# Kernel optimization log

Measured on AMD Instinct MI355X. Metric: run time of the kernel, lower is better.

Reference implementation:

```python
import jax, jax.numpy as jnp
import numpy as np

G, M, K = 4096, 50, 30          # graphs, nodes per graph, sort-pool k
H, NUM_LAYERS, F_IN = 32, 3, 128
DEG = 8
N = G * M
E = N * DEG
D_LAT = H * NUM_LAYERS + 1       # 97 = conv1d kernel/stride
DENSE_DIM = (((K - 2) // 2 + 1) - 5 + 1) * 32  # 352


def setup_inputs() -> dict:
    key = jax.random.key(0)
    ks = jax.random.split(key, 14)
    x = jax.random.normal(ks[0], (N, F_IN), dtype=jnp.float32)
    # graph-local random edges so each subgraph is self-contained
    offs = (jnp.arange(E, dtype=jnp.int32) // (M * DEG)) * M
    src = jax.random.randint(ks[1], (E,), 0, M, dtype=jnp.int32) + offs
    dst = jax.random.randint(ks[2], (E,), 0, M, dtype=jnp.int32) + offs
    edge_index = jnp.stack([src, dst])
    batch = jnp.repeat(jnp.arange(G, dtype=jnp.int32), M)

    def lin(k, i, o):
        return (jax.random.normal(k, (i, o), dtype=jnp.float32) / np.sqrt(i)).astype(jnp.float32)

    W0, b0 = lin(ks[3], F_IN, H), jnp.zeros((H,), jnp.float32)
    W1, b1 = lin(ks[4], H, H), jnp.zeros((H,), jnp.float32)
    W2, b2 = lin(ks[5], H, H), jnp.zeros((H,), jnp.float32)
    W3, b3 = lin(ks[6], H, 1), jnp.zeros((1,), jnp.float32)
    C1w = (jax.random.normal(ks[7], (16, 1, D_LAT)) / np.sqrt(D_LAT)).astype(jnp.float32)
    C1b = jnp.zeros((16,), jnp.float32)
    C2w = (jax.random.normal(ks[8], (32, 16, 5)) / np.sqrt(16 * 5)).astype(jnp.float32)
    C2b = jnp.zeros((32,), jnp.float32)
    L1w, L1b = lin(ks[9], DENSE_DIM, 128), jnp.zeros((128,), jnp.float32)
    L2w, L2b = lin(ks[10], 128, 1), jnp.zeros((1,), jnp.float32)
    return {"x": x, "edge_index": edge_index, "batch": batch,
            "W0": W0, "b0": b0, "W1": W1, "b1": b1, "W2": W2, "b2": b2,
            "W3": W3, "b3": b3, "C1w": C1w, "C1b": C1b, "C2w": C2w, "C2b": C2b,
            "L1w": L1w, "L1b": L1b, "L2w": L2w, "L2b": L2b}


def _gcn_norm(edge_index, n):
    # add self loops, symmetric normalization (PyG GCNConv default)
    loop = jnp.arange(n, dtype=edge_index.dtype)
    src = jnp.concatenate([edge_index[0], loop])
    dst = jnp.concatenate([edge_index[1], loop])
    deg = jax.ops.segment_sum(jnp.ones_like(dst, dtype=jnp.float32), dst, num_segments=n)
    dinv = jnp.where(deg > 0, deg ** -0.5, 0.0)
    return src, dst, dinv[src] * dinv[dst]


def _gcn_conv(h, W, b, src, dst, norm, n):
    h = h @ W                                    # [N, out]
    msg = h[src] * norm[:, None]                 # gather + weight
    return jax.ops.segment_sum(msg, dst, num_segments=n) + b


def reference(x, edge_index, batch, W0, b0, W1, b1, W2, b2, W3, b3,
              C1w, C1b, C2w, C2b, L1w, L1b, L2w, L2b):
    n = x.shape[0]
    src, dst, norm = _gcn_norm(edge_index, n)
    h1 = jnp.tanh(_gcn_conv(x, W0, b0, src, dst, norm, n))
    h2 = jnp.tanh(_gcn_conv(h1, W1, b1, src, dst, norm, n))
    h3 = jnp.tanh(_gcn_conv(h2, W2, b2, src, dst, norm, n))
    h4 = jnp.tanh(_gcn_conv(h3, W3, b3, src, dst, norm, n))
    lat = jnp.concatenate([h1, h2, h3, h4], axis=-1)      # [N, 97]
    # global_sort_pool: graphs are contiguous equal-size blocks (batch = arange(G).repeat(M)),
    # sort nodes within each graph by last channel, descending, keep top K
    xd = lat.reshape(G, M, D_LAT)
    order = jnp.argsort(-xd[..., -1], axis=1)             # [G, M]
    xs = jnp.take_along_axis(xd, order[..., None], axis=1)[:, :K]  # [G, K, 97]
    # Conv1d(1,16,97,stride=97) on [G,1,K*97] == per-slot linear over the 97 latent dims
    z = jnp.einsum('gtd,cd->gct', xs, C1w[:, 0, :]) + C1b[None, :, None]  # [G,16,K]
    z = jax.nn.relu(z)
    z = z.reshape(G, 16, K // 2, 2).max(axis=-1)          # MaxPool1d(2,2) -> [G,16,15]
    z = jax.lax.conv_general_dilated(z, C2w, window_strides=(1,), padding='VALID',
                                     dimension_numbers=('NCH', 'OIH', 'NCH'))
    z = jax.nn.relu(z + C2b[None, :, None])               # [G,32,11]
    z = z.reshape(G, -1)                                  # [G,352]
    z = jax.nn.relu(z @ L1w + L1b)
    # dropout: eval mode (identity)
    return z @ L2w + L2b                                  # [G,1]
```

## Files before the change

### kernel.cpp

```cpp
#include <hip/hip_runtime.h>
#include <math.h>

#define NG 4096
#define M 50
#define KTOP 30
#define H 32
#define F_IN 128
#define EPG 400
#define PADE 552
#define E_TOTAL (NG * EPG)
#define DLAT 97
#define LATS 100
#define NTHREADS 256
#define WS_C1P 0
#define XH 64

__device__ __forceinline__ float fast_tanh(float x) {
    x = fminf(fmaxf(x, -15.f), 15.f);
    float e = __expf(2.f * x);
    return 1.f - 2.f / (e + 1.f);
}

__global__ void prep_kernel(const float* __restrict__ C1w, float* __restrict__ ws) {
    const int tid = blockIdx.x * blockDim.x + threadIdx.x;
    if (tid < 1600) {
        int c = tid / 100, d = tid - c * 100;
        ws[WS_C1P + tid] = (d < DLAT) ? C1w[c * DLAT + d] : 0.f;
    }
}

template <int KIN>
__device__ __forceinline__ void gcn_matmul_acc(const float* hin, int istride,
                                               const float* __restrict__ W,
                                               const int* rows, float* acc, int j) {
#pragma unroll 2
    for (int k4 = 0; k4 < KIN / 4; k4++) {
        const float w0 = W[(4 * k4 + 0) * H + j];
        const float w1 = W[(4 * k4 + 1) * H + j];
        const float w2 = W[(4 * k4 + 2) * H + j];
        const float w3 = W[(4 * k4 + 3) * H + j];
#pragma unroll
        for (int r = 0; r < 7; r++) {
            const float4 xv = *(const float4*)(hin + rows[r] * istride + 4 * k4);
            acc[r] += xv.x * w0 + xv.y * w1 + xv.z * w2 + xv.w * w3;
        }
    }
}

template <int KIN>
__device__ __forceinline__ void gcn_matmul(const float* hin, int istride,
                                           const float* __restrict__ W,
                                           float (*tb)[H], int tid) {
    const int j = tid & 31, iset = tid >> 5;
    float acc[7];
    int rows[7];
#pragma unroll
    for (int r = 0; r < 7; r++) {
        acc[r] = 0.f;
        int i = iset + r * 8;
        rows[r] = (i >= M) ? (M - 1) : i;
    }
    gcn_matmul_acc<KIN>(hin, istride, W, rows, acc, j);
#pragma unroll
    for (int r = 0; r < 7; r++) {
        int i = iset + r * 8;
        if (i < M) tb[i][j] = acc[r];
    }
}

__device__ __forceinline__ void gcn_agg(const float (*tbuf)[H], const float* __restrict__ b,
                                        float (*lat)[LATS], int col0,
                                        const float* dinv, const unsigned short* csr_off,
                                        const unsigned char* csr_src, const float* csr_nrm,
                                        int tid) {
    const int j = tid & 31, iset = tid >> 5;
    for (int i = iset; i < M; i += 8) {
        float acc = tbuf[i][j] * dinv[i] * dinv[i];
        int e0 = csr_off[i], e1 = csr_off[i + 1];
        for (int e = e0; e < e1; e += 4) {
            unsigned sp = *(const unsigned*)(csr_src + e);
            float4 nr = *(const float4*)(csr_nrm + e);
            acc += tbuf[sp & 255][j] * nr.x;
            acc += tbuf[(sp >> 8) & 255][j] * nr.y;
            acc += tbuf[(sp >> 16) & 255][j] * nr.z;
            acc += tbuf[sp >> 24][j] * nr.w;
        }
        lat[i][col0 + j] = fast_tanh(acc + b[j]);
    }
}

struct Post {
    float pbuf[16][15];
    union {
        struct { float z1[16][KTOP]; unsigned char ord[52]; } a;
        struct { float z2[352]; float red[256]; } b;
    } u;
};

__global__ __launch_bounds__(NTHREADS, 4)
void dgcnn_kernel(const float* __restrict__ x, const int* __restrict__ eidx,
                  const float* __restrict__ ws,
                  const float* __restrict__ W0, const float* __restrict__ b0,
                  const float* __restrict__ W1, const float* __restrict__ b1,
                  const float* __restrict__ W2, const float* __restrict__ b2,
                  const float* __restrict__ W3, const float* __restrict__ b3,
                  const float* __restrict__ C1b,
                  const float* __restrict__ C2w, const float* __restrict__ C2b,
                  const float* __restrict__ L1w, const float* __restrict__ L1b,
                  const float* __restrict__ L2w, const float* __restrict__ L2b,
                  float* __restrict__ out) {
    __shared__ __align__(16) union Big {
        float xs[M][XH];
        float lat[M][LATS];
    } big;
    __shared__ __align__(16) union TP {
        float tbuf[M][H];
        Post post;
    } tp;
    __shared__ __align__(16) float csr_nrm[PADE];
    __shared__ unsigned char csr_src[PADE];
    __shared__ unsigned short csr_off[M + 2];
    __shared__ int   degi[M];
    __shared__ float dinv[M];

    const int g = blockIdx.x;
    const int tid = threadIdx.x;
    const int nbase = g * M;
    const int ebase = g * EPG;

    {
        const float4* xg4 = (const float4*)(x + (size_t)nbase * F_IN);
        float4* xs4 = (float4*)big.xs;
        for (int idx = tid; idx < M * XH / 4; idx += NTHREADS) {
            int i = idx >> 4, q = idx & 15;
            xs4[idx] = xg4[i * 32 + q];
        }
    }
    if (tid < M) degi[tid] = 1;
    for (int idx = tid; idx < PADE; idx += NTHREADS) {
        csr_nrm[idx] = 0.f;
        csr_src[idx] = 0;
    }
    __syncthreads();
    for (int e = tid; e < EPG; e += NTHREADS) {
        int d = eidx[E_TOTAL + ebase + e] - nbase;
        atomicAdd(&degi[d], 1);
    }
    __syncthreads();
    if (tid < M) dinv[tid] = rsqrtf((float)degi[tid]);
    if (tid < 64) {
        int cnt  = (tid < M) ? (degi[tid] - 1) : 0;
        int cntp = (cnt + 3) & ~3;
        int incl = cntp;
#pragma unroll
        for (int off = 1; off < 64; off <<= 1) {
            int nv = __shfl_up(incl, off);
            if (tid >= off) incl += nv;
        }
        if (tid < M) {
            csr_off[tid] = (unsigned short)(incl - cntp);
            degi[tid] = incl - cntp;
        }
        if (tid == M - 1) csr_off[M] = (unsigned short)incl;
    }
    __syncthreads();
    const int j1 = tid & 31, iset1 = tid >> 5;
    float acc1[7];
    int rows1[7];
#pragma unroll
    for (int r = 0; r < 7; r++) {
        acc1[r] = 0.f;
        int i = iset1 + r * 8;
        rows1[r] = (i >= M) ? (M - 1) : i;
    }
    for (int e = tid; e < EPG; e += NTHREADS) {
        int s = eidx[ebase + e] - nbase;
        int d = eidx[E_TOTAL + ebase + e] - nbase;
        float nr = dinv[s] * dinv[d];
        int pos = atomicAdd(&degi[d], 1);
        csr_src[pos] = (unsigned char)s;
        csr_nrm[pos] = nr;
    }
    gcn_matmul_acc<XH>(&big.xs[0][0], XH, W0, rows1, acc1, j1);
    __syncthreads();
    {
        const float4* xg4 = (const float4*)(x + (size_t)nbase * F_IN);
        float4* xs4 = (float4*)big.xs;
        for (int idx = tid; idx < M * XH / 4; idx += NTHREADS) {
            int i = idx >> 4, q = idx & 15;
            xs4[idx] = xg4[i * 32 + 16 + q];
        }
    }
    __syncthreads();
    gcn_matmul_acc<XH>(&big.xs[0][0], XH, W0 + XH * H, rows1, acc1, j1);
#pragma unroll
    for (int r = 0; r < 7; r++) {
        int i = iset1 + r * 8;
        if (i < M) tp.tbuf[i][j1] = acc1[r];
    }
    __syncthreads();

    gcn_agg(tp.tbuf, b0, big.lat, 0, dinv, csr_off, csr_src, csr_nrm, tid);
    for (int idx = tid; idx < 3 * M; idx += NTHREADS)
        big.lat[idx / 3][DLAT + idx % 3] = 0.f;
    __syncthreads();
    gcn_matmul<H>(&big.lat[0][0], LATS, W1, tp.tbuf, tid);
    __syncthreads();
    gcn_agg(tp.tbuf, b1, big.lat, 32, dinv, csr_off, csr_src, csr_nrm, tid);
    __syncthreads();
    gcn_matmul<H>(&big.lat[0][32], LATS, W2, tp.tbuf, tid);
    __syncthreads();
    gcn_agg(tp.tbuf, b2, big.lat, 64, dinv, csr_off, csr_src, csr_nrm, tid);
    __syncthreads();
    if (tid < M) {
        float acc = 0.f;
        for (int k = 0; k < H; k++) acc += big.lat[tid][64 + k] * W3[k];
        tp.tbuf[tid][0] = acc;
    }
    __syncthreads();
    if (tid < M) {
        float acc = tp.tbuf[tid][0] * dinv[tid] * dinv[tid];
        int e0 = csr_off[tid], e1 = csr_off[tid + 1];
        for (int e = e0; e < e1; e += 4) {
            unsigned sp = *(const unsigned*)(csr_src + e);
            float4 nr = *(const float4*)(csr_nrm + e);
            acc += tp.tbuf[sp & 255][0] * nr.x + tp.tbuf[(sp >> 8) & 255][0] * nr.y
                 + tp.tbuf[(sp >> 16) & 255][0] * nr.z + tp.tbuf[sp >> 24][0] * nr.w;
        }
        big.lat[tid][96] = tanhf(acc + b3[0]);
    }
    __syncthreads();

    if (tid < M) {
        float v = big.lat[tid][96];
        int r = 0;
        for (int jj = 0; jj < M; jj++) {
            float vj = big.lat[jj][96];
            r += (vj > v) || (vj == v && jj < tid);
        }
        tp.post.u.a.ord[r] = (unsigned char)tid;
    }
    __syncthreads();

    for (int idx = tid; idx < 16 * KTOP; idx += NTHREADS) {
        int t = idx >> 4, c = idx & 15;
        const float4* row = (const float4*)big.lat[tp.post.u.a.ord[t]];
        const float4* cw  = (const float4*)(ws + WS_C1P + c * LATS);
        float acc = 0.f;
#pragma unroll 5
        for (int q = 0; q < LATS / 4; q++) {
            float4 rv = row[q], wv = cw[q];
            acc += rv.x * wv.x + rv.y * wv.y + rv.z * wv.z + rv.w * wv.w;
        }
        tp.post.u.a.z1[c][t] = fmaxf(acc + C1b[c], 0.f);
    }
    __syncthreads();

    for (int idx = tid; idx < 16 * 15; idx += NTHREADS) {
        int c = idx / 15, t = idx - c * 15;
        tp.post.pbuf[c][t] = fmaxf(tp.post.u.a.z1[c][2 * t],
                                   tp.post.u.a.z1[c][2 * t + 1]);
    }
    __syncthreads();

    for (int idx = tid; idx < 352; idx += NTHREADS) {
        int o = idx / 11, t = idx - o * 11;
        float acc = C2b[o];
        for (int i = 0; i < 16; i++) {
#pragma unroll
            for (int k = 0; k < 5; k++)
                acc += tp.post.pbuf[i][t + k] * C2w[(o * 16 + i) * 5 + k];
        }
        tp.post.u.b.z2[idx] = fmaxf(acc, 0.f);
    }
    __syncthreads();

    {
        int jj = tid & 127, half = tid >> 7;
        float acc = (half == 0) ? L1b[jj] : 0.f;
        int f0 = half * 176;
        for (int f = f0; f < f0 + 176; f++)
            acc += tp.post.u.b.z2[f] * L1w[f * 128 + jj];
        tp.post.u.b.red[tid] = acc;
    }
    __syncthreads();
    if (tid < 128)
        tp.post.u.b.red[tid] =
            fmaxf(tp.post.u.b.red[tid] + tp.post.u.b.red[tid + 128], 0.f)
            * L2w[tid];
    __syncthreads();
    if (tid < 64) {
        float v = tp.post.u.b.red[tid] + tp.post.u.b.red[tid + 64];
#pragma unroll
        for (int off = 32; off >= 1; off >>= 1)
            v += __shfl_down(v, off);
        if (tid == 0) out[g] = v + L2b[0];
    }
}

extern "C" void kernel_launch(void* const* d_in, const int* in_sizes, int n_in,
                              void* d_out, int out_size, void* d_ws, size_t ws_size,
                              hipStream_t stream) {
    const float* x    = (const float*)d_in[0];
    const int*   eidx = (const int*)d_in[1];
    float* ws = (float*)d_ws;
    prep_kernel<<<7, 256, 0, stream>>>((const float*)d_in[11], ws);
    dgcnn_kernel<<<NG, NTHREADS, 0, stream>>>(
        x, eidx, ws,
        (const float*)d_in[3],  (const float*)d_in[4],
        (const float*)d_in[5],  (const float*)d_in[6],
        (const float*)d_in[7],  (const float*)d_in[8],
        (const float*)d_in[9],  (const float*)d_in[10],
        (const float*)d_in[12],
        (const float*)d_in[13], (const float*)d_in[14],
        (const float*)d_in[15], (const float*)d_in[16],
        (const float*)d_in[17], (const float*)d_in[18],
        (float*)d_out);
}
```

Measured before the change: 376.7 us.

## Factor GCN normalization into row scaling and drop per-edge norm array

Rewrites the symmetric GCN normalization so each source row is pre-scaled by dinv after the matmul and the aggregated sum is scaled by dinv of the destination. This removes the per-edge csr_nrm shared array, its initialization and float4 loads, and the per-edge multiplies in aggregation. Padding edges now point to an extra zero row (index 50) of tbuf, which enlarges tbuf by one row. Rounding order changes slightly.

```diff
diff --git a/kernel.cpp b/kernel.cpp
--- a/kernel.cpp
+++ b/kernel.cpp
@@ -50,7 +50,7 @@
 template <int KIN>
 __device__ __forceinline__ void gcn_matmul(const float* hin, int istride,
                                            const float* __restrict__ W,
-                                           float (*tb)[H], int tid) {
+                                           float (*tb)[H], const float* dinv, int tid) {
     const int j = tid & 31, iset = tid >> 5;
     float acc[7];
     int rows[7];
@@ -64,28 +64,26 @@
 #pragma unroll
     for (int r = 0; r < 7; r++) {
         int i = iset + r * 8;
-        if (i < M) tb[i][j] = acc[r];
+        if (i < M) tb[i][j] = acc[r] * dinv[i];
     }
 }
 
 __device__ __forceinline__ void gcn_agg(const float (*tbuf)[H], const float* __restrict__ b,
                                         float (*lat)[LATS], int col0,
                                         const float* dinv, const unsigned short* csr_off,
-                                        const unsigned char* csr_src, const float* csr_nrm,
-                                        int tid) {
+                                        const unsigned char* csr_src, int tid) {
     const int j = tid & 31, iset = tid >> 5;
     for (int i = iset; i < M; i += 8) {
-        float acc = tbuf[i][j] * dinv[i] * dinv[i];
+        float acc = tbuf[i][j];
         int e0 = csr_off[i], e1 = csr_off[i + 1];
         for (int e = e0; e < e1; e += 4) {
             unsigned sp = *(const unsigned*)(csr_src + e);
-            float4 nr = *(const float4*)(csr_nrm + e);
-            acc += tbuf[sp & 255][j] * nr.x;
-            acc += tbuf[(sp >> 8) & 255][j] * nr.y;
-            acc += tbuf[(sp >> 16) & 255][j] * nr.z;
-            acc += tbuf[sp >> 24][j] * nr.w;
-        }
-        lat[i][col0 + j] = fast_tanh(acc + b[j]);
+            acc += tbuf[sp & 255][j];
+            acc += tbuf[(sp >> 8) & 255][j];
+            acc += tbuf[(sp >> 16) & 255][j];
+            acc += tbuf[sp >> 24][j];
+        }
+        lat[i][col0 + j] = fast_tanh(acc * dinv[i] + b[j]);
     }
 }
 
@@ -114,10 +112,9 @@
         float lat[M][LATS];
     } big;
     __shared__ __align__(16) union TP {
-        float tbuf[M][H];
+        float tbuf[M + 1][H];
         Post post;
     } tp;
-    __shared__ __align__(16) float csr_nrm[PADE];
     __shared__ unsigned char csr_src[PADE];
     __shared__ unsigned short csr_off[M + 2];
     __shared__ int   degi[M];
@@ -137,10 +134,8 @@
         }
     }
     if (tid < M) degi[tid] = 1;
-    for (int idx = tid; idx < PADE; idx += NTHREADS) {
-        csr_nrm[idx] = 0.f;
-        csr_src[idx] = 0;
-    }
+    for (int idx = tid; idx < PADE / 4; idx += NTHREADS)
+        ((unsigned*)csr_src)[idx] = 0x32323232u;
     __syncthreads();
     for (int e = tid; e < EPG; e += NTHREADS) {
         int d = eidx[E_TOTAL + ebase + e] - nbase;
@@ -176,10 +171,8 @@
     for (int e = tid; e < EPG; e += NTHREADS) {
         int s = eidx[ebase + e] - nbase;
         int d = eidx[E_TOTAL + ebase + e] - nbase;
-        float nr = dinv[s] * dinv[d];
         int pos = atomicAdd(&degi[d], 1);
         csr_src[pos] = (unsigned char)s;
-        csr_nrm[pos] = nr;
     }
     gcn_matmul_acc<XH>(&big.xs[0][0], XH, W0, rows1, acc1, j1);
     __syncthreads();
@@ -196,38 +189,38 @@
 #pragma unroll
     for (int r = 0; r < 7; r++) {
         int i = iset1 + r * 8;
-        if (i < M) tp.tbuf[i][j1] = acc1[r];
-    }
-    __syncthreads();
-
-    gcn_agg(tp.tbuf, b0, big.lat, 0, dinv, csr_off, csr_src, csr_nrm, tid);
+        if (i < M) tp.tbuf[i][j1] = acc1[r] * dinv[i];
+    }
+    if (tid < H) tp.tbuf[M][tid] = 0.f;
+    __syncthreads();
+
+    gcn_agg(tp.tbuf, b0, big.lat, 0, dinv, csr_off, csr_src, tid);
     for (int idx = tid; idx < 3 * M; idx += NTHREADS)
         big.lat[idx / 3][DLAT + idx % 3] = 0.f;
     __syncthreads();
-    gcn_matmul<H>(&big.lat[0][0], LATS, W1, tp.tbuf, tid);
-    __syncthreads();
-    gcn_agg(tp.tbuf, b1, big.lat, 32, dinv, csr_off, csr_src, csr_nrm, tid);
-    __syncthreads();
-    gcn_matmul<H>(&big.lat[0][32], LATS, W2, tp.tbuf, tid);
-    __syncthreads();
-    gcn_agg(tp.tbuf, b2, big.lat, 64, dinv, csr_off, csr_src, csr_nrm, tid);
+    gcn_matmul<H>(&big.lat[0][0], LATS, W1, tp.tbuf, dinv, tid);
+    __syncthreads();
+    gcn_agg(tp.tbuf, b1, big.lat, 32, dinv, csr_off, csr_src, tid);
+    __syncthreads();
+    gcn_matmul<H>(&big.lat[0][32], LATS, W2, tp.tbuf, dinv, tid);
+    __syncthreads();
+    gcn_agg(tp.tbuf, b2, big.lat, 64, dinv, csr_off, csr_src, tid);
     __syncthreads();
     if (tid < M) {
         float acc = 0.f;
         for (int k = 0; k < H; k++) acc += big.lat[tid][64 + k] * W3[k];
-        tp.tbuf[tid][0] = acc;
+        tp.tbuf[tid][0] = acc * dinv[tid];
     }
     __syncthreads();
     if (tid < M) {
-        float acc = tp.tbuf[tid][0] * dinv[tid] * dinv[tid];
+        float acc = tp.tbuf[tid][0];
         int e0 = csr_off[tid], e1 = csr_off[tid + 1];
         for (int e = e0; e < e1; e += 4) {
             unsigned sp = *(const unsigned*)(csr_src + e);
-            float4 nr = *(const float4*)(csr_nrm + e);
-            acc += tp.tbuf[sp & 255][0] * nr.x + tp.tbuf[(sp >> 8) & 255][0] * nr.y
-                 + tp.tbuf[(sp >> 16) & 255][0] * nr.z + tp.tbuf[sp >> 24][0] * nr.w;
-        }
-        big.lat[tid][96] = tanhf(acc + b3[0]);
+            acc += tp.tbuf[sp & 255][0] + tp.tbuf[(sp >> 8) & 255][0]
+                 + tp.tbuf[(sp >> 16) & 255][0] + tp.tbuf[sp >> 24][0];
+        }
+        big.lat[tid][96] = tanhf(acc * dinv[tid] + b3[0]);
     }
     __syncthreads();
 
```

After: 377.5 us. Within noise of the previous version (+0.2%).
